# Kernel optimization log

Hardware: AMD Instinct MI355X
Metric: run time of the kernel (lower is better)

The kernel has to match this reference:

```python
import jax, jax.numpy as jnp
import numpy as np

B, S, D = 2, 2048, 512
H = 8
G = 4
LAMBDA_INIT = 0.2  # 0.8 - 0.6*exp(-0.3*(layer_idx-1)) with layer_idx=1
EPS = 1e-5


def setup_inputs() -> dict:
    key = jax.random.key(0)
    ks = jax.random.split(key, 16)
    n = jax.random.normal
    return {
        "x": n(ks[0], (B, S, D), jnp.float32),
        "K1_w": n(ks[1], (D, D), jnp.float32) * 0.02,
        "K1_b": n(ks[2], (D,), jnp.float32) * 0.02,
        "Q1_w": n(ks[3], (D, D), jnp.float32) * 0.02,
        "K2_w": n(ks[4], (D, D), jnp.float32) * 0.02,
        "K2_b": n(ks[5], (D,), jnp.float32) * 0.02,
        "Q2_w": n(ks[6], (D, D), jnp.float32) * 0.02,
        "V_w": n(ks[7], (D, D), jnp.float32) * 0.02,
        "lambda_q1": n(ks[8], (H, 1), jnp.float32),
        "lambda_k1": n(ks[9], (H, 1), jnp.float32),
        "lambda_q2": n(ks[10], (H, 1), jnp.float32),
        "lambda_k2": n(ks[11], (H, 1), jnp.float32),
        "gn_w": jnp.ones((D,), jnp.float32),
        "gn_b": jnp.zeros((D,), jnp.float32),
        "out_w": n(ks[12], (D, D), jnp.float32) * 0.02,
        "out_b": n(ks[13], (D,), jnp.float32) * 0.02,
    }


def reference(x, K1_w, K1_b, Q1_w, K2_w, K2_b, Q2_w, V_w,
              lambda_q1, lambda_k1, lambda_q2, lambda_k2,
              gn_w, gn_b, out_w, out_b):
    b, s, d = x.shape
    hd = d // H

    def heads(t):  # (b,s,d) -> (b,H,s,hd)
        return t.reshape(b, s, H, hd).transpose(0, 2, 1, 3)

    q1 = heads(x @ Q1_w.T)
    k1 = heads(x @ K1_w.T + K1_b)
    q2 = heads(x @ Q2_w.T)
    k2 = heads(x @ K2_w.T + K2_b)
    v = heads(x @ V_w.T)

    scale = hd ** 0.5
    a1 = jax.nn.softmax(jnp.einsum('bhqd,bhkd->bhqk', q1, k1) / scale, axis=-1)
    a2 = jax.nn.softmax(jnp.einsum('bhqd,bhkd->bhqk', q2, k2) / scale, axis=-1)

    lam = (jnp.exp(lambda_q1 * lambda_k1)
           - jnp.exp(lambda_q2 * lambda_k2) + LAMBDA_INIT)  # (H,1)
    attn = a1 - lam.reshape(1, H, 1, 1) * a2

    o = jnp.einsum('bhqk,bhkd->bhqd', attn, v)
    o = o.transpose(0, 2, 1, 3).reshape(b, s, d)

    # GroupNorm over channels: input (b, d, s), groups G normalize over (d/G, s)
    xc = o.transpose(0, 2, 1).reshape(b, G, d // G, s)
    mu = xc.mean(axis=(2, 3), keepdims=True)
    var = xc.var(axis=(2, 3), keepdims=True)
    xn = ((xc - mu) * jax.lax.rsqrt(var + EPS)).reshape(b, d, s)
    xn = xn * gn_w[None, :, None] + gn_b[None, :, None]

    y = xn.transpose(0, 2, 1) @ out_w.T + out_b
    return y
```

## Files before the change

### kernel.cpp

```cpp
#include <hip/hip_runtime.h>
#include <hip/hip_bf16.h>

typedef __bf16 bf16;
typedef __attribute__((ext_vector_type(8))) __bf16 bf16x8;
typedef __attribute__((ext_vector_type(4))) float f32x4;

#define MFMA16(a, b, c) __builtin_amdgcn_mfma_f32_16x16x32_bf16((a), (b), (c), 0, 0, 0)

static constexpr float EPS = 1e-5f;
static constexpr float LAMBDA_INIT = 0.2f;

__device__ __forceinline__ bf16x8 cvt8(const float* p) {
    const f32x4 a = *(const f32x4*)p;
    const f32x4 b = *(const f32x4*)(p + 4);
    bf16x8 r;
    r[0] = (bf16)a[0]; r[1] = (bf16)a[1]; r[2] = (bf16)a[2]; r[3] = (bf16)a[3];
    r[4] = (bf16)b[0]; r[5] = (bf16)b[1]; r[6] = (bf16)b[2]; r[7] = (bf16)b[3];
    return r;
}

__device__ __forceinline__ void gload_lds16(const void* g, void* l) {
    __builtin_amdgcn_global_load_lds(
        (const __attribute__((address_space(1))) unsigned int*)g,
        (__attribute__((address_space(3))) unsigned int*)l,
        16, 0, 0);
}

__global__ __launch_bounds__(256) void proj_kernel(
    const float* __restrict__ x,
    const float* __restrict__ q1w, const float* __restrict__ k1w,
    const float* __restrict__ q2w, const float* __restrict__ k2w,
    const float* __restrict__ vw,
    const float* __restrict__ k1b, const float* __restrict__ k2b,
    bf16* __restrict__ q1o, bf16* __restrict__ k1o,
    bf16* __restrict__ q2o, bf16* __restrict__ k2o,
    bf16* __restrict__ vto)
{
    __shared__ __align__(16) float As[128 * 32];
    __shared__ __align__(16) float Bs[128 * 32];

    const int tid = threadIdx.x;
    const int wave = tid >> 6, lane = tid & 63;
    const int l15 = lane & 15, quad = lane >> 4;
    const int wm = wave >> 1, wn = wave & 1;

    const int mb = blockIdx.x / 20;
    const int nb = blockIdx.x % 20;
    const int wsel = nb >> 2;
    const int nrow0 = (nb & 3) * 128;

    const float* W = (wsel == 0) ? q1w : (wsel == 1) ? k1w :
                     (wsel == 2) ? q2w : (wsel == 3) ? k2w : vw;

    const int srow = lane >> 3;
    const int scol = (lane & 7) * 4;
    const float* xg = x + (size_t)(mb * 128 + srow) * 512 + scol;
    const float* wg = W + (size_t)(nrow0 + srow) * 512 + scol;

    f32x4 acc[4][4];
#pragma unroll
    for (int i = 0; i < 4; ++i)
#pragma unroll
        for (int j = 0; j < 4; ++j)
            acc[i][j] = (f32x4){0.f, 0.f, 0.f, 0.f};

    for (int k0 = 0; k0 < 512; k0 += 32) {
#pragma unroll
        for (int c = 0; c < 4; ++c) {
            const int chunk = wave * 4 + c;
            gload_lds16(xg + (size_t)(chunk * 8) * 512 + k0, As + chunk * 256);
            gload_lds16(wg + (size_t)(chunk * 8) * 512 + k0, Bs + chunk * 256);
        }
        __syncthreads();

        bf16x8 af[4], bfr[4];
#pragma unroll
        for (int i = 0; i < 4; ++i)
            af[i] = cvt8(As + (wm * 64 + i * 16 + l15) * 32 + quad * 8);
#pragma unroll
        for (int j = 0; j < 4; ++j)
            bfr[j] = cvt8(Bs + (wn * 64 + j * 16 + l15) * 32 + quad * 8);

#pragma unroll
        for (int i = 0; i < 4; ++i)
#pragma unroll
            for (int j = 0; j < 4; ++j)
                acc[i][j] = MFMA16(af[i], bfr[j], acc[i][j]);

        __syncthreads();
    }

    const float scale = (wsel == 0 || wsel == 2) ? 0.125f : 1.0f;
#pragma unroll
    for (int j = 0; j < 4; ++j) {
        const int ncol = nrow0 + wn * 64 + j * 16 + l15;
        float bias = 0.f;
        if (wsel == 1) bias = k1b[ncol];
        if (wsel == 3) bias = k2b[ncol];
        const int h = ncol >> 6, hd = ncol & 63;
#pragma unroll
        for (int i = 0; i < 4; ++i) {
#pragma unroll
            for (int r = 0; r < 4; ++r) {
                const int m = mb * 128 + wm * 64 + i * 16 + quad * 4 + r;
                const int bidx = m >> 11, s = m & 2047;
                const float v = acc[i][j][r] * scale + bias;
                if (wsel == 4) {
                    const int s5 = s & 31;
                    const int p = ((s5 & 15) >> 2) * 8 + (s5 & 3) + ((s5 >> 4) << 2);
                    const int sp = (s & ~31) | p;
                    vto[((size_t)(bidx * 8 + h) * 64 + hd) * 2048 + sp] = (bf16)v;
                } else {
                    bf16* dst = (wsel == 0) ? q1o : (wsel == 1) ? k1o :
                                (wsel == 2) ? q2o : k2o;
                    dst[((size_t)(bidx * 8 + h) * 2048 + s) * 64 + hd] = (bf16)v;
                }
            }
        }
    }
}

__global__ __launch_bounds__(512, 4) void attn_kernel(
    const bf16* __restrict__ q1, const bf16* __restrict__ k1,
    const bf16* __restrict__ q2, const bf16* __restrict__ k2,
    const bf16* __restrict__ vt,
    const float* __restrict__ lq1, const float* __restrict__ lk1,
    const float* __restrict__ lq2, const float* __restrict__ lk2,
    bf16* __restrict__ o, float* __restrict__ stats)
{
    __shared__ __align__(16) bf16 smem[12288];
    __shared__ float lbuf[8][2][16];
    __shared__ float sred[8][2];

    const int tid = threadIdx.x;
    const int wave = tid >> 6;
    const int lane = tid & 63;
    const int l15 = lane & 15, quad = lane >> 4;
    const int qtile = wave & 3;
    const int kg = wave >> 2;

    const int bh = blockIdx.x >> 5;
    const int qt = blockIdx.x & 31;
    const int b = bh >> 3, h = bh & 7;

    const bf16* k1t = k1 + (size_t)bh * 2048 * 64;
    const bf16* k2t = k2 + (size_t)bh * 2048 * 64;
    const bf16* vtt = vt + (size_t)bh * 64 * 2048;

    const int qrow = qt * 64 + qtile * 16 + l15;
    const bf16* q1p = q1 + ((size_t)bh * 2048 + qrow) * 64 + quad * 8;
    const bf16* q2p = q2 + ((size_t)bh * 2048 + qrow) * 64 + quad * 8;
    const bf16x8 q1f0 = *(const bf16x8*)(q1p);
    const bf16x8 q1f1 = *(const bf16x8*)(q1p + 32);
    const bf16x8 q2f0 = *(const bf16x8*)(q2p);
    const bf16x8 q2f1 = *(const bf16x8*)(q2p + 32);

    const int sw = wave & 3;
    const int skey0 = (wave < 4) ? 0 : 1024;
    bf16* k1dst = smem + wave * 512;
    bf16* k2dst = smem + 4096 + wave * 512;
    bf16* vdst  = smem + 8192 + wave * 512;
    const size_t ksrc0 = (size_t)(skey0 + sw * 8 + (lane >> 3)) * 64
                       + 8 * ((lane & 7) ^ (lane >> 3));
    const size_t vsrc0 = (size_t)(sw * 16 + (lane >> 2)) * 2048 + skey0 + (lane & 3) * 8;

    const bf16* k1r = smem + kg * 2048;
    const bf16* k2r = smem + 4096 + kg * 2048;
    const bf16* vr  = smem + 8192 + kg * 2048;

    const int koffa = 8 * (quad ^ (l15 & 7));
    const int koffb = 8 * ((quad + 4) ^ (l15 & 7));

    f32x4 O1[4], O2[4];
    float l1 = 0.f, l2 = 0.f;
#pragma unroll
    for (int t = 0; t < 4; ++t) {
        O1[t] = (f32x4){0.f, 0.f, 0.f, 0.f};
        O2[t] = (f32x4){0.f, 0.f, 0.f, 0.f};
    }

    for (int it = 0; it < 32; ++it) {
        const size_t koff = ksrc0 + (size_t)it * 32 * 64;
        gload_lds16(k1t + koff, k1dst);
        gload_lds16(k2t + koff, k2dst);
        gload_lds16(vtt + vsrc0 + it * 32, vdst);
        __syncthreads();

        const bf16x8 k1t0a = *(const bf16x8*)(k1r + l15 * 64 + koffa);
        const bf16x8 k1t0b = *(const bf16x8*)(k1r + l15 * 64 + koffb);
        const bf16x8 k1t1a = *(const bf16x8*)(k1r + (16 + l15) * 64 + koffa);
        const bf16x8 k1t1b = *(const bf16x8*)(k1r + (16 + l15) * 64 + koffb);
        const bf16x8 k2t0a = *(const bf16x8*)(k2r + l15 * 64 + koffa);
        const bf16x8 k2t0b = *(const bf16x8*)(k2r + l15 * 64 + koffb);
        const bf16x8 k2t1a = *(const bf16x8*)(k2r + (16 + l15) * 64 + koffa);
        const bf16x8 k2t1b = *(const bf16x8*)(k2r + (16 + l15) * 64 + koffb);
        const bf16x8 v0 = *(const bf16x8*)(vr + l15 * 32 + quad * 8);
        const bf16x8 v1 = *(const bf16x8*)(vr + (16 + l15) * 32 + quad * 8);
        const bf16x8 v2 = *(const bf16x8*)(vr + (32 + l15) * 32 + quad * 8);
        const bf16x8 v3 = *(const bf16x8*)(vr + (48 + l15) * 32 + quad * 8);

        f32x4 z = (f32x4){0.f, 0.f, 0.f, 0.f};
        f32x4 s1t0 = MFMA16(k1t0a, q1f0, z);  s1t0 = MFMA16(k1t0b, q1f1, s1t0);
        f32x4 s1t1 = MFMA16(k1t1a, q1f0, z);  s1t1 = MFMA16(k1t1b, q1f1, s1t1);
        f32x4 s2t0 = MFMA16(k2t0a, q2f0, z);  s2t0 = MFMA16(k2t0b, q2f1, s2t0);
        f32x4 s2t1 = MFMA16(k2t1a, q2f0, z);  s2t1 = MFMA16(k2t1b, q2f1, s2t1);

        bf16x8 b1, b2;
#pragma unroll
        for (int r = 0; r < 4; ++r) {
            float e;
            e = __expf(s1t0[r]); l1 += e; b1[r]     = (bf16)e;
            e = __expf(s1t1[r]); l1 += e; b1[4 + r] = (bf16)e;
            e = __expf(s2t0[r]); l2 += e; b2[r]     = (bf16)e;
            e = __expf(s2t1[r]); l2 += e; b2[4 + r] = (bf16)e;
        }

        O1[0] = MFMA16(v0, b1, O1[0]);
        O1[1] = MFMA16(v1, b1, O1[1]);
        O1[2] = MFMA16(v2, b1, O1[2]);
        O1[3] = MFMA16(v3, b1, O1[3]);
        O2[0] = MFMA16(v0, b2, O2[0]);
        O2[1] = MFMA16(v1, b2, O2[1]);
        O2[2] = MFMA16(v2, b2, O2[2]);
        O2[3] = MFMA16(v3, b2, O2[3]);

        __syncthreads();
    }

    l1 += __shfl_xor(l1, 16, 64);  l1 += __shfl_xor(l1, 32, 64);
    l2 += __shfl_xor(l2, 16, 64);  l2 += __shfl_xor(l2, 32, 64);
    if (lane < 16) {
        lbuf[wave][0][lane] = l1;
        lbuf[wave][1][lane] = l2;
    }
    __syncthreads();

    f32x4* rb = (f32x4*)smem;
    if (wave == 4 || wave == 5) {
        f32x4* dst = rb + (wave - 4) * 512;
#pragma unroll
        for (int t = 0; t < 4; ++t) {
            dst[t * 64 + lane]       = O1[t];
            dst[(4 + t) * 64 + lane] = O2[t];
        }
    }
    __syncthreads();
    if (wave == 0 || wave == 1) {
        const f32x4* src = rb + wave * 512;
#pragma unroll
        for (int t = 0; t < 4; ++t) {
            O1[t] += src[t * 64 + lane];
            O2[t] += src[(4 + t) * 64 + lane];
        }
    }
    __syncthreads();
    if (wave == 6 || wave == 7) {
        f32x4* dst = rb + (wave - 6) * 512;
#pragma unroll
        for (int t = 0; t < 4; ++t) {
            dst[t * 64 + lane]       = O1[t];
            dst[(4 + t) * 64 + lane] = O2[t];
        }
    }
    __syncthreads();
    if (wave == 2 || wave == 3) {
        const f32x4* src = rb + (wave - 2) * 512;
#pragma unroll
        for (int t = 0; t < 4; ++t) {
            O1[t] += src[t * 64 + lane];
            O2[t] += src[(4 + t) * 64 + lane];
        }
    }

    float ssum = 0.f, ssq = 0.f;
    if (wave < 4) {
        const float L1 = l1 + lbuf[wave + 4][0][l15];
        const float L2 = l2 + lbuf[wave + 4][1][l15];
        const float lam = __expf(lq1[h] * lk1[h]) - __expf(lq2[h] * lk2[h]) + LAMBDA_INIT;
        const float inv1 = 1.f / L1;
        const float inv2 = lam / L2;
        const size_t row = (size_t)(b * 2048 + qt * 64 + wave * 16 + l15) * 512 + h * 64;
#pragma unroll
        for (int t = 0; t < 4; ++t) {
#pragma unroll
            for (int r = 0; r < 4; ++r) {
                const float val = O1[t][r] * inv1 - O2[t][r] * inv2;
                ssum += val;
                ssq += val * val;
                o[row + t * 16 + quad * 4 + r] = (bf16)val;
            }
        }
    }
#pragma unroll
    for (int off = 1; off < 64; off <<= 1) {
        ssum += __shfl_xor(ssum, off, 64);
        ssq += __shfl_xor(ssq, off, 64);
    }
    if (lane == 0) { sred[wave][0] = ssum; sred[wave][1] = ssq; }
    __syncthreads();
    if (tid == 0) {
        float s0 = 0.f, s1 = 0.f;
        for (int w = 0; w < 8; ++w) { s0 += sred[w][0]; s1 += sred[w][1]; }
        const int bg = b * 4 + (h >> 1);
        atomicAdd(&stats[bg * 2], s0);
        atomicAdd(&stats[bg * 2 + 1], s1);
    }
}

__global__ __launch_bounds__(256) void prep_kernel(
    const float* __restrict__ ow, const float* __restrict__ gnw,
    const float* __restrict__ gnb, bf16* __restrict__ owg,
    float* __restrict__ S0)
{
    __shared__ float red[4];
    const int tid = threadIdx.x;
    const int n0 = blockIdx.x * 16;
    const int c0 = tid, c1 = tid + 256;

    const float gw0 = gnw[c0], gw1 = gnw[c1];
    const float gb0 = gnb[c0], gb1 = gnb[c1];

    for (int n = 0; n < 16; ++n) {
        const size_t rowb = (size_t)(n0 + n) * 512;
        const float w0 = ow[rowb + c0];
        const float w1 = ow[rowb + c1];
        owg[rowb + c0] = (bf16)(w0 * gw0);
        owg[rowb + c1] = (bf16)(w1 * gw1);
        float s = gb0 * w0 + gb1 * w1;
#pragma unroll
        for (int off = 1; off < 64; off <<= 1) s += __shfl_xor(s, off, 64);
        if ((tid & 63) == 0) red[tid >> 6] = s;
        __syncthreads();
        if (tid == 0) S0[n0 + n] = red[0] + red[1] + red[2] + red[3];
        __syncthreads();
    }
}

__global__ __launch_bounds__(256) void out_gemm_kernel(
    const bf16* __restrict__ o, const bf16* __restrict__ owg,
    const float* __restrict__ S0, const float* __restrict__ stats,
    const float* __restrict__ ob, float* __restrict__ y)
{
    __shared__ __align__(16) bf16 As[64 * 32];
    __shared__ __align__(16) bf16 Bs[64 * 32];

    const int tid = threadIdx.x;
    const int wave = tid >> 6, lane = tid & 63;
    const int l15 = lane & 15, quad = lane >> 4;

    const int mb = blockIdx.x >> 3;
    const int nb = blockIdx.x & 7;
    const int b = mb >> 5;

    const float N = 128.f * 2048.f;
    float mu[4], rs[4];
#pragma unroll
    for (int g = 0; g < 4; ++g) {
        const float m = stats[(b * 4 + g) * 2] / N;
        const float var = stats[(b * 4 + g) * 2 + 1] / N - m * m;
        mu[g] = m;
        rs[g] = rsqrtf(var + EPS);
    }

    const int srow = wave * 16 + (lane >> 2);
    const int scol = (lane & 3) * 8;
    const bf16* ag = o + (size_t)(mb * 64 + srow) * 512 + scol;
    const bf16* bg = owg + (size_t)(nb * 64 + srow) * 512 + scol;
    bf16* adst = As + wave * 512;
    bf16* bdst = Bs + wave * 512;

    f32x4 acc[4], tot[4];
#pragma unroll
    for (int i = 0; i < 4; ++i) {
        acc[i] = (f32x4){0.f, 0.f, 0.f, 0.f};
        tot[i] = (f32x4){0.f, 0.f, 0.f, 0.f};
    }
    float s1g[4];
    float s1p = 0.f;
#pragma unroll
    for (int g = 0; g < 4; ++g) s1g[g] = 0.f;

    for (int kk = 0; kk < 16; ++kk) {
        gload_lds16(ag + kk * 32, adst);
        gload_lds16(bg + kk * 32, bdst);
        __syncthreads();

        bf16x8 af[4];
#pragma unroll
        for (int i = 0; i < 4; ++i)
            af[i] = *(const bf16x8*)(As + (i * 16 + l15) * 32 + quad * 8);
        const bf16x8 bf = *(const bf16x8*)(Bs + (wave * 16 + l15) * 32 + quad * 8);

#pragma unroll
        for (int i = 0; i < 4; ++i)
            acc[i] = MFMA16(af[i], bf, acc[i]);

#pragma unroll
        for (int j = 0; j < 8; ++j) s1p += (float)bf[j];

        __syncthreads();

        if ((kk & 3) == 3) {
            const int g = kk >> 2;
#pragma unroll
            for (int i = 0; i < 4; ++i) {
#pragma unroll
                for (int r = 0; r < 4; ++r) tot[i][r] += rs[g] * acc[i][r];
                acc[i] = (f32x4){0.f, 0.f, 0.f, 0.f};
            }
            float sg = s1p + __shfl_xor(s1p, 16, 64);
            sg += __shfl_xor(sg, 32, 64);
            s1g[g] = sg;
            s1p = 0.f;
        }
    }

    const int ncol = nb * 64 + wave * 16 + l15;
    float bias = S0[ncol] + ob[ncol];
#pragma unroll
    for (int g = 0; g < 4; ++g) bias -= mu[g] * rs[g] * s1g[g];

#pragma unroll
    for (int i = 0; i < 4; ++i) {
#pragma unroll
        for (int r = 0; r < 4; ++r) {
            const int m = mb * 64 + i * 16 + quad * 4 + r;
            y[(size_t)m * 512 + ncol] = tot[i][r] + bias;
        }
    }
}

extern "C" void kernel_launch(void* const* d_in, const int* in_sizes, int n_in,
                              void* d_out, int out_size, void* d_ws, size_t ws_size,
                              hipStream_t stream)
{
    const float* x   = (const float*)d_in[0];
    const float* K1w = (const float*)d_in[1];
    const float* K1b = (const float*)d_in[2];
    const float* Q1w = (const float*)d_in[3];
    const float* K2w = (const float*)d_in[4];
    const float* K2b = (const float*)d_in[5];
    const float* Q2w = (const float*)d_in[6];
    const float* Vw  = (const float*)d_in[7];
    const float* lq1 = (const float*)d_in[8];
    const float* lk1 = (const float*)d_in[9];
    const float* lq2 = (const float*)d_in[10];
    const float* lk2 = (const float*)d_in[11];
    const float* gnw = (const float*)d_in[12];
    const float* gnb = (const float*)d_in[13];
    const float* Ow  = (const float*)d_in[14];
    const float* Ob  = (const float*)d_in[15];

    const size_t SZ = (size_t)2 * 8 * 2048 * 64;
    bf16* q1 = (bf16*)d_ws;
    bf16* k1 = q1 + SZ;
    bf16* q2 = k1 + SZ;
    bf16* k2 = q2 + SZ;
    bf16* vt = k2 + SZ;
    bf16* o  = vt + SZ;
    bf16* owg = o + SZ;
    float* S0 = (float*)(owg + 512 * 512);
    float* stats = S0 + 512;

    hipMemsetAsync(stats, 0, 16 * sizeof(float), stream);

    proj_kernel<<<640, 256, 0, stream>>>(x, Q1w, K1w, Q2w, K2w, Vw, K1b, K2b,
                                         q1, k1, q2, k2, vt);
    prep_kernel<<<32, 256, 0, stream>>>(Ow, gnw, gnb, owg, S0);
    attn_kernel<<<512, 512, 0, stream>>>(q1, k1, q2, k2, vt,
                                         lq1, lk1, lq2, lk2, o, stats);
    out_gemm_kernel<<<512, 256, 0, stream>>>(o, owg, S0, stats, Ob,
                                             (float*)d_out);
}
```

Baseline: 200.4 us.

## Give each attention wave two query tiles with larger key chunks per iteration

Each attention wave now handles two 16-row query tiles and one quarter of a 128-key chunk, instead of one query tile and half of a 64-key chunk. Every K/V fragment read from LDS is reused across both query tiles, and the loop runs 16 iterations instead of 32, so there are half as many barriers. The cost is a larger LDS buffer, more registers and a lower occupancy hint, plus a deeper reduction across four key-split waves at the end. The stats memset is also folded into prep_kernel, removing one extra launch.

```diff
diff --git a/kernel.cpp b/kernel.cpp
--- a/kernel.cpp
+++ b/kernel.cpp
@@ -120,7 +120,7 @@
     }
 }
 
-__global__ __launch_bounds__(512, 4) void attn_kernel(
+__global__ __launch_bounds__(512, 2) void attn_kernel(
     const bf16* __restrict__ q1, const bf16* __restrict__ k1,
     const bf16* __restrict__ q2, const bf16* __restrict__ k2,
     const bf16* __restrict__ vt,
@@ -128,16 +128,16 @@
     const float* __restrict__ lq2, const float* __restrict__ lk2,
     bf16* __restrict__ o, float* __restrict__ stats)
 {
-    __shared__ __align__(16) bf16 smem[12288];
-    __shared__ float lbuf[8][2][16];
-    __shared__ float sred[8][2];
+    __shared__ __align__(16) bf16 smem[32768];
+    __shared__ float lbuf[8][2][2][16];
+    __shared__ float sred[2][2];
 
     const int tid = threadIdx.x;
     const int wave = tid >> 6;
     const int lane = tid & 63;
     const int l15 = lane & 15, quad = lane >> 4;
-    const int qtile = wave & 3;
-    const int kg = wave >> 2;
+    const int qh = wave >> 2;
+    const int kq = wave & 3;
 
     const int bh = blockIdx.x >> 5;
     const int qt = blockIdx.x & 31;
@@ -147,43 +147,62 @@
     const bf16* k2t = k2 + (size_t)bh * 2048 * 64;
     const bf16* vtt = vt + (size_t)bh * 64 * 2048;
 
-    const int qrow = qt * 64 + qtile * 16 + l15;
-    const bf16* q1p = q1 + ((size_t)bh * 2048 + qrow) * 64 + quad * 8;
-    const bf16* q2p = q2 + ((size_t)bh * 2048 + qrow) * 64 + quad * 8;
-    const bf16x8 q1f0 = *(const bf16x8*)(q1p);
-    const bf16x8 q1f1 = *(const bf16x8*)(q1p + 32);
-    const bf16x8 q2f0 = *(const bf16x8*)(q2p);
-    const bf16x8 q2f1 = *(const bf16x8*)(q2p + 32);
-
-    const int sw = wave & 3;
-    const int skey0 = (wave < 4) ? 0 : 1024;
-    bf16* k1dst = smem + wave * 512;
-    bf16* k2dst = smem + 4096 + wave * 512;
-    bf16* vdst  = smem + 8192 + wave * 512;
-    const size_t ksrc0 = (size_t)(skey0 + sw * 8 + (lane >> 3)) * 64
-                       + 8 * ((lane & 7) ^ (lane >> 3));
-    const size_t vsrc0 = (size_t)(sw * 16 + (lane >> 2)) * 2048 + skey0 + (lane & 3) * 8;
-
-    const bf16* k1r = smem + kg * 2048;
-    const bf16* k2r = smem + 4096 + kg * 2048;
-    const bf16* vr  = smem + 8192 + kg * 2048;
-
+    bf16x8 q1f0[2], q1f1[2], q2f0[2], q2f1[2];
+#pragma unroll
+    for (int t = 0; t < 2; ++t) {
+        const int qrow = qt * 64 + (qh * 2 + t) * 16 + l15;
+        const bf16* q1p = q1 + ((size_t)bh * 2048 + qrow) * 64 + quad * 8;
+        const bf16* q2p = q2 + ((size_t)bh * 2048 + qrow) * 64 + quad * 8;
+        q1f0[t] = *(const bf16x8*)(q1p);
+        q1f1[t] = *(const bf16x8*)(q1p + 32);
+        q2f0[t] = *(const bf16x8*)(q2p);
+        q2f1[t] = *(const bf16x8*)(q2p + 32);
+    }
+
+    const bf16* gsrc[6]; bf16* ldst[6]; int gstep[6];
+#pragma unroll
+    for (int j = 0; j < 6; ++j) {
+        const int c = wave * 6 + j;
+        if (c < 16) {
+            gsrc[j] = k1t + (size_t)(c * 8 + (lane >> 3)) * 64
+                    + 8 * ((lane & 7) ^ (lane >> 3));
+            ldst[j] = smem + c * 512;
+            gstep[j] = 128 * 64;
+        } else if (c < 32) {
+            const int i = c - 16;
+            gsrc[j] = k2t + (size_t)(i * 8 + (lane >> 3)) * 64
+                    + 8 * ((lane & 7) ^ (lane >> 3));
+            ldst[j] = smem + 8192 + i * 512;
+            gstep[j] = 128 * 64;
+        } else {
+            const int i = c - 32;
+            gsrc[j] = vtt + (size_t)((i & 3) * 16 + (lane >> 2)) * 2048
+                    + (i >> 2) * 32 + (lane & 3) * 8;
+            ldst[j] = smem + 16384 + i * 512;
+            gstep[j] = 128;
+        }
+    }
+
+    const bf16* k1r = smem + kq * 2048;
+    const bf16* k2r = smem + 8192 + kq * 2048;
+    const bf16* vr  = smem + 16384 + kq * 2048;
     const int koffa = 8 * (quad ^ (l15 & 7));
     const int koffb = 8 * ((quad + 4) ^ (l15 & 7));
 
-    f32x4 O1[4], O2[4];
-    float l1 = 0.f, l2 = 0.f;
-#pragma unroll
-    for (int t = 0; t < 4; ++t) {
-        O1[t] = (f32x4){0.f, 0.f, 0.f, 0.f};
-        O2[t] = (f32x4){0.f, 0.f, 0.f, 0.f};
-    }
-
-    for (int it = 0; it < 32; ++it) {
-        const size_t koff = ksrc0 + (size_t)it * 32 * 64;
-        gload_lds16(k1t + koff, k1dst);
-        gload_lds16(k2t + koff, k2dst);
-        gload_lds16(vtt + vsrc0 + it * 32, vdst);
+    f32x4 O1[2][4], O2[2][4];
+    float l1[2] = {0.f, 0.f}, l2[2] = {0.f, 0.f};
+#pragma unroll
+    for (int t = 0; t < 2; ++t)
+#pragma unroll
+        for (int r = 0; r < 4; ++r) {
+            O1[t][r] = (f32x4){0.f, 0.f, 0.f, 0.f};
+            O2[t][r] = (f32x4){0.f, 0.f, 0.f, 0.f};
+        }
+
+    for (int it = 0; it < 16; ++it) {
+#pragma unroll
+        for (int j = 0; j < 6; ++j)
+            gload_lds16(gsrc[j] + (size_t)it * gstep[j], ldst[j]);
         __syncthreads();
 
         const bf16x8 k1t0a = *(const bf16x8*)(k1r + l15 * 64 + koffa);
@@ -199,96 +218,110 @@
         const bf16x8 v2 = *(const bf16x8*)(vr + (32 + l15) * 32 + quad * 8);
         const bf16x8 v3 = *(const bf16x8*)(vr + (48 + l15) * 32 + quad * 8);
 
-        f32x4 z = (f32x4){0.f, 0.f, 0.f, 0.f};
-        f32x4 s1t0 = MFMA16(k1t0a, q1f0, z);  s1t0 = MFMA16(k1t0b, q1f1, s1t0);
-        f32x4 s1t1 = MFMA16(k1t1a, q1f0, z);  s1t1 = MFMA16(k1t1b, q1f1, s1t1);
-        f32x4 s2t0 = MFMA16(k2t0a, q2f0, z);  s2t0 = MFMA16(k2t0b, q2f1, s2t0);
-        f32x4 s2t1 = MFMA16(k2t1a, q2f0, z);  s2t1 = MFMA16(k2t1b, q2f1, s2t1);
-
-        bf16x8 b1, b2;
-#pragma unroll
-        for (int r = 0; r < 4; ++r) {
-            float e;
-            e = __expf(s1t0[r]); l1 += e; b1[r]     = (bf16)e;
-            e = __expf(s1t1[r]); l1 += e; b1[4 + r] = (bf16)e;
-            e = __expf(s2t0[r]); l2 += e; b2[r]     = (bf16)e;
-            e = __expf(s2t1[r]); l2 += e; b2[4 + r] = (bf16)e;
-        }
-
-        O1[0] = MFMA16(v0, b1, O1[0]);
-        O1[1] = MFMA16(v1, b1, O1[1]);
-        O1[2] = MFMA16(v2, b1, O1[2]);
-        O1[3] = MFMA16(v3, b1, O1[3]);
-        O2[0] = MFMA16(v0, b2, O2[0]);
-        O2[1] = MFMA16(v1, b2, O2[1]);
-        O2[2] = MFMA16(v2, b2, O2[2]);
-        O2[3] = MFMA16(v3, b2, O2[3]);
-
-        __syncthreads();
-    }
-
-    l1 += __shfl_xor(l1, 16, 64);  l1 += __shfl_xor(l1, 32, 64);
-    l2 += __shfl_xor(l2, 16, 64);  l2 += __shfl_xor(l2, 32, 64);
+#pragma unroll
+        for (int t = 0; t < 2; ++t) {
+            f32x4 z = (f32x4){0.f, 0.f, 0.f, 0.f};
+            f32x4 s1t0 = MFMA16(k1t0a, q1f0[t], z);  s1t0 = MFMA16(k1t0b, q1f1[t], s1t0);
+            f32x4 s1t1 = MFMA16(k1t1a, q1f0[t], z);  s1t1 = MFMA16(k1t1b, q1f1[t], s1t1);
+            f32x4 s2t0 = MFMA16(k2t0a, q2f0[t], z);  s2t0 = MFMA16(k2t0b, q2f1[t], s2t0);
+            f32x4 s2t1 = MFMA16(k2t1a, q2f0[t], z);  s2t1 = MFMA16(k2t1b, q2f1[t], s2t1);
+
+            bf16x8 b1, b2;
+#pragma unroll
+            for (int r = 0; r < 4; ++r) {
+                float e;
+                e = __expf(s1t0[r]); l1[t] += e; b1[r]     = (bf16)e;
+                e = __expf(s1t1[r]); l1[t] += e; b1[4 + r] = (bf16)e;
+                e = __expf(s2t0[r]); l2[t] += e; b2[r]     = (bf16)e;
+                e = __expf(s2t1[r]); l2[t] += e; b2[4 + r] = (bf16)e;
+            }
+
+            O1[t][0] = MFMA16(v0, b1, O1[t][0]);
+            O1[t][1] = MFMA16(v1, b1, O1[t][1]);
+            O1[t][2] = MFMA16(v2, b1, O1[t][2]);
+            O1[t][3] = MFMA16(v3, b1, O1[t][3]);
+            O2[t][0] = MFMA16(v0, b2, O2[t][0]);
+            O2[t][1] = MFMA16(v1, b2, O2[t][1]);
+            O2[t][2] = MFMA16(v2, b2, O2[t][2]);
+            O2[t][3] = MFMA16(v3, b2, O2[t][3]);
+        }
+
+        __syncthreads();
+    }
+
+#pragma unroll
+    for (int t = 0; t < 2; ++t) {
+        l1[t] += __shfl_xor(l1[t], 16, 64);  l1[t] += __shfl_xor(l1[t], 32, 64);
+        l2[t] += __shfl_xor(l2[t], 16, 64);  l2[t] += __shfl_xor(l2[t], 32, 64);
+    }
     if (lane < 16) {
-        lbuf[wave][0][lane] = l1;
-        lbuf[wave][1][lane] = l2;
+        lbuf[wave][0][0][lane] = l1[0];  lbuf[wave][0][1][lane] = l1[1];
+        lbuf[wave][1][0][lane] = l2[0];  lbuf[wave][1][1][lane] = l2[1];
+    }
+
+    f32x4* rb = (f32x4*)smem;
+    if (kq & 1) {
+        f32x4* dst = rb + (wave >> 1) * 1024;
+#pragma unroll
+        for (int t = 0; t < 2; ++t)
+#pragma unroll
+            for (int r = 0; r < 4; ++r) {
+                dst[(t * 8 + r) * 64 + lane]     = O1[t][r];
+                dst[(t * 8 + 4 + r) * 64 + lane] = O2[t][r];
+            }
     }
     __syncthreads();
-
-    f32x4* rb = (f32x4*)smem;
-    if (wave == 4 || wave == 5) {
-        f32x4* dst = rb + (wave - 4) * 512;
-#pragma unroll
-        for (int t = 0; t < 4; ++t) {
-            dst[t * 64 + lane]       = O1[t];
-            dst[(4 + t) * 64 + lane] = O2[t];
-        }
+    if (!(kq & 1)) {
+        const f32x4* src = rb + (wave >> 1) * 1024;
+#pragma unroll
+        for (int t = 0; t < 2; ++t)
+#pragma unroll
+            for (int r = 0; r < 4; ++r) {
+                O1[t][r] += src[(t * 8 + r) * 64 + lane];
+                O2[t][r] += src[(t * 8 + 4 + r) * 64 + lane];
+            }
     }
     __syncthreads();
-    if (wave == 0 || wave == 1) {
-        const f32x4* src = rb + wave * 512;
-#pragma unroll
-        for (int t = 0; t < 4; ++t) {
-            O1[t] += src[t * 64 + lane];
-            O2[t] += src[(4 + t) * 64 + lane];
-        }
+    if (kq == 2) {
+        f32x4* dst = rb + (wave >> 2) * 1024;
+#pragma unroll
+        for (int t = 0; t < 2; ++t)
+#pragma unroll
+            for (int r = 0; r < 4; ++r) {
+                dst[(t * 8 + r) * 64 + lane]     = O1[t][r];
+                dst[(t * 8 + 4 + r) * 64 + lane] = O2[t][r];
+            }
     }
     __syncthreads();
-    if (wave == 6 || wave == 7) {
-        f32x4* dst = rb + (wave - 6) * 512;
-#pragma unroll
-        for (int t = 0; t < 4; ++t) {
-            dst[t * 64 + lane]       = O1[t];
-            dst[(4 + t) * 64 + lane] = O2[t];
-        }
-    }
-    __syncthreads();
-    if (wave == 2 || wave == 3) {
-        const f32x4* src = rb + (wave - 2) * 512;
-#pragma unroll
-        for (int t = 0; t < 4; ++t) {
-            O1[t] += src[t * 64 + lane];
-            O2[t] += src[(4 + t) * 64 + lane];
-        }
-    }
 
     float ssum = 0.f, ssq = 0.f;
-    if (wave < 4) {
-        const float L1 = l1 + lbuf[wave + 4][0][l15];
-        const float L2 = l2 + lbuf[wave + 4][1][l15];
+    if (kq == 0) {
+        const f32x4* src = rb + (wave >> 2) * 1024;
         const float lam = __expf(lq1[h] * lk1[h]) - __expf(lq2[h] * lk2[h]) + LAMBDA_INIT;
-        const float inv1 = 1.f / L1;
-        const float inv2 = lam / L2;
-        const size_t row = (size_t)(b * 2048 + qt * 64 + wave * 16 + l15) * 512 + h * 64;
-#pragma unroll
-        for (int t = 0; t < 4; ++t) {
+#pragma unroll
+        for (int t = 0; t < 2; ++t) {
 #pragma unroll
             for (int r = 0; r < 4; ++r) {
-                const float val = O1[t][r] * inv1 - O2[t][r] * inv2;
-                ssum += val;
-                ssq += val * val;
-                o[row + t * 16 + quad * 4 + r] = (bf16)val;
-            }
+                O1[t][r] += src[(t * 8 + r) * 64 + lane];
+                O2[t][r] += src[(t * 8 + 4 + r) * 64 + lane];
+            }
+            const float L1 = lbuf[qh * 4][0][t][l15] + lbuf[qh * 4 + 1][0][t][l15]
+                           + lbuf[qh * 4 + 2][0][t][l15] + lbuf[qh * 4 + 3][0][t][l15];
+            const float L2 = lbuf[qh * 4][1][t][l15] + lbuf[qh * 4 + 1][1][t][l15]
+                           + lbuf[qh * 4 + 2][1][t][l15] + lbuf[qh * 4 + 3][1][t][l15];
+            const float inv1 = 1.f / L1;
+            const float inv2 = lam / L2;
+            const size_t row = (size_t)(b * 2048 + qt * 64 + (qh * 2 + t) * 16 + l15) * 512
+                             + h * 64;
+#pragma unroll
+            for (int tr = 0; tr < 4; ++tr)
+#pragma unroll
+                for (int r = 0; r < 4; ++r) {
+                    const float val = O1[t][tr][r] * inv1 - O2[t][tr][r] * inv2;
+                    ssum += val;
+                    ssq += val * val;
+                    o[row + tr * 16 + quad * 4 + r] = (bf16)val;
+                }
         }
     }
 #pragma unroll
@@ -296,24 +329,24 @@
         ssum += __shfl_xor(ssum, off, 64);
         ssq += __shfl_xor(ssq, off, 64);
     }
-    if (lane == 0) { sred[wave][0] = ssum; sred[wave][1] = ssq; }
+    if (kq == 0 && lane == 0) { sred[qh][0] = ssum; sred[qh][1] = ssq; }
     __syncthreads();
     if (tid == 0) {
-        float s0 = 0.f, s1 = 0.f;
-        for (int w = 0; w < 8; ++w) { s0 += sred[w][0]; s1 += sred[w][1]; }
         const int bg = b * 4 + (h >> 1);
-        atomicAdd(&stats[bg * 2], s0);
-        atomicAdd(&stats[bg * 2 + 1], s1);
+        atomicAdd(&stats[bg * 2],     sred[0][0] + sred[1][0]);
+        atomicAdd(&stats[bg * 2 + 1], sred[0][1] + sred[1][1]);
     }
 }
 
 __global__ __launch_bounds__(256) void prep_kernel(
     const float* __restrict__ ow, const float* __restrict__ gnw,
     const float* __restrict__ gnb, bf16* __restrict__ owg,
-    float* __restrict__ S0)
+    float* __restrict__ S0, float* __restrict__ stats)
 {
     __shared__ float red[4];
     const int tid = threadIdx.x;
+    if (blockIdx.x == 0 && tid < 16) stats[tid] = 0.f;
+
     const int n0 = blockIdx.x * 16;
     const int c0 = tid, c1 = tid + 256;
 
@@ -462,11 +495,9 @@
     float* S0 = (float*)(owg + 512 * 512);
     float* stats = S0 + 512;
 
-    hipMemsetAsync(stats, 0, 16 * sizeof(float), stream);
-
     proj_kernel<<<640, 256, 0, stream>>>(x, Q1w, K1w, Q2w, K2w, Vw, K1b, K2b,
                                          q1, k1, q2, k2, vt);
-    prep_kernel<<<32, 256, 0, stream>>>(Ow, gnw, gnb, owg, S0);
+    prep_kernel<<<32, 256, 0, stream>>>(Ow, gnw, gnb, owg, S0, stats);
     attn_kernel<<<512, 512, 0, stream>>>(q1, k1, q2, k2, vt,
                                          lq1, lk1, lq2, lk2, o, stats);
     out_gemm_kernel<<<512, 256, 0, stream>>>(o, owg, S0, stats, Ob,
```

After: 218.4 us. 9.0% more time.

## Pre-convert x and projection weights to bf16 in a merged prep kernel

Applied to the files above, without the earlier changes.

Adds a conversion pass to the prep kernel that casts x and the five projection weight matrices to bf16 in the workspace. The projection GEMM now stages bf16 tiles in LDS and reads them directly as MFMA operands instead of converting fp32 per tile, which halves LDS footprint and global traffic per tile. The memset of the stats buffer is folded into the prep kernel and the old prep work is merged into the same launch, removing one launch. The trade-off is an extra full read and write pass over x and the weights before the GEMM. xb reuses the o buffer, which is not written until the attention kernel.

```diff
diff --git a/kernel.cpp b/kernel.cpp
--- a/kernel.cpp
+++ b/kernel.cpp
@@ -26,18 +26,66 @@
         16, 0, 0);
 }
 
-__global__ __launch_bounds__(256) void proj_kernel(
+__global__ __launch_bounds__(256) void prep_kernel(
     const float* __restrict__ x,
     const float* __restrict__ q1w, const float* __restrict__ k1w,
     const float* __restrict__ q2w, const float* __restrict__ k2w,
     const float* __restrict__ vw,
+    const float* __restrict__ ow, const float* __restrict__ gnw,
+    const float* __restrict__ gnb,
+    bf16* __restrict__ xb, bf16* __restrict__ wb,
+    bf16* __restrict__ owg, float* __restrict__ S0, float* __restrict__ stats)
+{
+    const int tid = threadIdx.x;
+    if (blockIdx.x < 1664) {
+        const size_t base = ((size_t)blockIdx.x * 256 + tid) * 8;
+        if (base < 2097152) {
+            *(bf16x8*)(xb + base) = cvt8(x + base);
+        } else {
+            const size_t wbase = base - 2097152;
+            const int wsel = (int)(wbase >> 18);
+            const size_t off = wbase & 262143;
+            const float* W = (wsel == 0) ? q1w : (wsel == 1) ? k1w :
+                             (wsel == 2) ? q2w : (wsel == 3) ? k2w : vw;
+            *(bf16x8*)(wb + wbase) = cvt8(W + off);
+        }
+        return;
+    }
+
+    __shared__ float red[4];
+    const int pb = blockIdx.x - 1664;
+    if (pb == 0 && tid < 16) stats[tid] = 0.f;
+
+    const int n0 = pb * 16;
+    const int c0 = tid, c1 = tid + 256;
+    const float gw0 = gnw[c0], gw1 = gnw[c1];
+    const float gb0 = gnb[c0], gb1 = gnb[c1];
+
+    for (int n = 0; n < 16; ++n) {
+        const size_t rowb = (size_t)(n0 + n) * 512;
+        const float w0 = ow[rowb + c0];
+        const float w1 = ow[rowb + c1];
+        owg[rowb + c0] = (bf16)(w0 * gw0);
+        owg[rowb + c1] = (bf16)(w1 * gw1);
+        float s = gb0 * w0 + gb1 * w1;
+#pragma unroll
+        for (int off = 1; off < 64; off <<= 1) s += __shfl_xor(s, off, 64);
+        if ((tid & 63) == 0) red[tid >> 6] = s;
+        __syncthreads();
+        if (tid == 0) S0[n0 + n] = red[0] + red[1] + red[2] + red[3];
+        __syncthreads();
+    }
+}
+
+__global__ __launch_bounds__(256) void proj_kernel(
+    const bf16* __restrict__ xb, const bf16* __restrict__ wb,
     const float* __restrict__ k1b, const float* __restrict__ k2b,
     bf16* __restrict__ q1o, bf16* __restrict__ k1o,
     bf16* __restrict__ q2o, bf16* __restrict__ k2o,
     bf16* __restrict__ vto)
 {
-    __shared__ __align__(16) float As[128 * 32];
-    __shared__ __align__(16) float Bs[128 * 32];
+    __shared__ __align__(16) bf16 As[128 * 32];
+    __shared__ __align__(16) bf16 Bs[128 * 32];
 
     const int tid = threadIdx.x;
     const int wave = tid >> 6, lane = tid & 63;
@@ -49,13 +97,10 @@
     const int wsel = nb >> 2;
     const int nrow0 = (nb & 3) * 128;
 
-    const float* W = (wsel == 0) ? q1w : (wsel == 1) ? k1w :
-                     (wsel == 2) ? q2w : (wsel == 3) ? k2w : vw;
-
-    const int srow = lane >> 3;
-    const int scol = (lane & 7) * 4;
-    const float* xg = x + (size_t)(mb * 128 + srow) * 512 + scol;
-    const float* wg = W + (size_t)(nrow0 + srow) * 512 + scol;
+    const int srow = lane >> 2;
+    const int scol = (lane & 3) * 8;
+    const bf16* ag = xb + (size_t)(mb * 128 + srow) * 512 + scol;
+    const bf16* bg = wb + (size_t)(wsel * 512 + nrow0 + srow) * 512 + scol;
 
     f32x4 acc[4][4];
 #pragma unroll
@@ -66,20 +111,20 @@
 
     for (int k0 = 0; k0 < 512; k0 += 32) {
 #pragma unroll
-        for (int c = 0; c < 4; ++c) {
-            const int chunk = wave * 4 + c;
-            gload_lds16(xg + (size_t)(chunk * 8) * 512 + k0, As + chunk * 256);
-            gload_lds16(wg + (size_t)(chunk * 8) * 512 + k0, Bs + chunk * 256);
+        for (int c = 0; c < 2; ++c) {
+            const int chunk = wave * 2 + c;
+            gload_lds16(ag + (size_t)(chunk * 16) * 512 + k0, As + chunk * 512);
+            gload_lds16(bg + (size_t)(chunk * 16) * 512 + k0, Bs + chunk * 512);
         }
         __syncthreads();
 
         bf16x8 af[4], bfr[4];
 #pragma unroll
         for (int i = 0; i < 4; ++i)
-            af[i] = cvt8(As + (wm * 64 + i * 16 + l15) * 32 + quad * 8);
+            af[i] = *(const bf16x8*)(As + (wm * 64 + i * 16 + l15) * 32 + quad * 8);
 #pragma unroll
         for (int j = 0; j < 4; ++j)
-            bfr[j] = cvt8(Bs + (wn * 64 + j * 16 + l15) * 32 + quad * 8);
+            bfr[j] = *(const bf16x8*)(Bs + (wn * 64 + j * 16 + l15) * 32 + quad * 8);
 
 #pragma unroll
         for (int i = 0; i < 4; ++i)
@@ -304,35 +349,6 @@
         const int bg = b * 4 + (h >> 1);
         atomicAdd(&stats[bg * 2], s0);
         atomicAdd(&stats[bg * 2 + 1], s1);
-    }
-}
-
-__global__ __launch_bounds__(256) void prep_kernel(
-    const float* __restrict__ ow, const float* __restrict__ gnw,
-    const float* __restrict__ gnb, bf16* __restrict__ owg,
-    float* __restrict__ S0)
-{
-    __shared__ float red[4];
-    const int tid = threadIdx.x;
-    const int n0 = blockIdx.x * 16;
-    const int c0 = tid, c1 = tid + 256;
-
-    const float gw0 = gnw[c0], gw1 = gnw[c1];
-    const float gb0 = gnb[c0], gb1 = gnb[c1];
-
-    for (int n = 0; n < 16; ++n) {
-        const size_t rowb = (size_t)(n0 + n) * 512;
-        const float w0 = ow[rowb + c0];
-        const float w1 = ow[rowb + c1];
-        owg[rowb + c0] = (bf16)(w0 * gw0);
-        owg[rowb + c1] = (bf16)(w1 * gw1);
-        float s = gb0 * w0 + gb1 * w1;
-#pragma unroll
-        for (int off = 1; off < 64; off <<= 1) s += __shfl_xor(s, off, 64);
-        if ((tid & 63) == 0) red[tid >> 6] = s;
-        __syncthreads();
-        if (tid == 0) S0[n0 + n] = red[0] + red[1] + red[2] + red[3];
-        __syncthreads();
     }
 }
 
@@ -458,15 +474,16 @@
     bf16* k2 = q2 + SZ;
     bf16* vt = k2 + SZ;
     bf16* o  = vt + SZ;
-    bf16* owg = o + SZ;
+    bf16* xb = o;
+    bf16* wb = o + SZ;
+    bf16* owg = wb + (size_t)2560 * 512;
     float* S0 = (float*)(owg + 512 * 512);
     float* stats = S0 + 512;
 
-    hipMemsetAsync(stats, 0, 16 * sizeof(float), stream);
-
-    proj_kernel<<<640, 256, 0, stream>>>(x, Q1w, K1w, Q2w, K2w, Vw, K1b, K2b,
+    prep_kernel<<<1696, 256, 0, stream>>>(x, Q1w, K1w, Q2w, K2w, Vw,
+                                          Ow, gnw, gnb, xb, wb, owg, S0, stats);
+    proj_kernel<<<640, 256, 0, stream>>>(xb, wb, K1b, K2b,
                                          q1, k1, q2, k2, vt);
-    prep_kernel<<<32, 256, 0, stream>>>(Ow, gnw, gnb, owg, S0);
     attn_kernel<<<512, 512, 0, stream>>>(q1, k1, q2, k2, vt,
                                          lq1, lk1, lq2, lk2, o, stats);
     out_gemm_kernel<<<512, 256, 0, stream>>>(o, owg, S0, stats, Ob,
```

Result: faster. 190.2 us (-5.1%).
